# Performance work log

Measured on AMD Instinct MI355X. Metric: run time of the kernel, lower is better.

## Reference

```python
import jax, jax.numpy as jnp
import numpy as np

HID = 2048
HEADS = 16
HD = HID // HEADS  # 128
EPS = 1e-6


def setup_inputs() -> dict:
    key = jax.random.key(0)
    ks = jax.random.split(key, 9)
    s = 1.0 / np.sqrt(HID)
    return {
        "hidden_states": jax.random.normal(ks[0], (4, 4096, HID), jnp.float32),
        "q_w": jax.random.normal(ks[1], (HID, HID), jnp.float32) * s,
        "q_b": jnp.zeros((HID,), jnp.float32),
        "k_w": jax.random.normal(ks[2], (HID, HID), jnp.float32) * s,
        "k_b": jnp.zeros((HID,), jnp.float32),
        "v_w": jax.random.normal(ks[3], (HID, HID), jnp.float32) * s,
        "v_b": jnp.zeros((HID,), jnp.float32),
        "o_w": jax.random.normal(ks[4], (HID, HID), jnp.float32) * s,
        "o_b": jnp.zeros((HID,), jnp.float32),
    }


def _heads(x, b, s):
    # [B,S,HID] -> [B,H,S,Dh]
    return x.reshape(b, s, HEADS, HD).transpose(0, 2, 1, 3)


def reference(hidden_states, q_w, q_b, k_w, k_b, v_w, v_b, o_w, o_b):
    b, s, _ = hidden_states.shape
    # torch Linear: y = x @ W.T + b
    q = _heads(hidden_states @ q_w.T + q_b, b, s)
    k = _heads(hidden_states @ k_w.T + k_b, b, s)
    v = _heads(hidden_states @ v_w.T + v_b, b, s)
    # kernel feature map: elu(x) + 1
    qp = jax.nn.elu(q) + 1.0
    kp = jax.nn.elu(k) + 1.0
    # KV outer-product reduction over sequence: [B,H,Dh,Dh]
    kv = jnp.einsum('bhsd,bhse->bhde', kp, v)
    # normalizer z = q' @ sum_s k'  -> [B,H,S,1]
    z = jnp.einsum('bhsd,bhd->bhs', qp, kp.sum(axis=2))[..., None]
    attn = jnp.einsum('bhsd,bhde->bhse', qp, kv) / (z + EPS)
    out = attn.transpose(0, 2, 1, 3).reshape(b, s, HID)
    return out @ o_w.T + o_b
```

## Files before the change

### kernel.cpp

```cpp
#include <hip/hip_runtime.h>
#include <hip/hip_bf16.h>

#define HIDC 2048
#define NHEADS 16
#define HDIM 128
#define NB 4
#define NS 4096
#define NROWS (NB*NS)
#define QSTR 6144
#define EPSV 1e-6f

typedef __attribute__((ext_vector_type(8))) short s16x8;
typedef __attribute__((ext_vector_type(4))) float f32x4;
typedef __attribute__((ext_vector_type(16))) float f32x16;
typedef __attribute__((ext_vector_type(8))) unsigned short u16x8;

static __device__ __forceinline__ unsigned short f2b(float f) {
  unsigned int u = __float_as_uint(f);
  u += 0x7fffu + ((u >> 16) & 1u);
  return (unsigned short)(u >> 16);
}
static __device__ __forceinline__ float b2f(unsigned short h) {
  return __uint_as_float(((unsigned int)h) << 16);
}

static __device__ __forceinline__ void gload_lds16(const unsigned short* g, unsigned short* l) {
  __builtin_amdgcn_global_load_lds(
      (const __attribute__((address_space(1))) void*)g,
      (__attribute__((address_space(3))) void*)l, 16, 0, 0);
}

__global__ __launch_bounds__(256) void convert_all(
    const float* __restrict__ hs, const float* __restrict__ qw,
    const float* __restrict__ kw, const float* __restrict__ vw,
    const float* __restrict__ ow,
    unsigned short* __restrict__ hsb, unsigned short* __restrict__ qwb,
    unsigned short* __restrict__ kwb, unsigned short* __restrict__ vwb,
    unsigned short* __restrict__ owb)
{
  int bid = blockIdx.x;
  const float* src; unsigned short* dst; size_t base;
  if (bid < 16384) { src = hs; dst = hsb; base = (size_t)bid << 11; }
  else {
    int t = bid - 16384; int wsel = t >> 11; int wb = t & 2047;
    src = wsel == 0 ? qw : wsel == 1 ? kw : wsel == 2 ? vw : ow;
    dst = wsel == 0 ? qwb : wsel == 1 ? kwb : wsel == 2 ? vwb : owb;
    base = (size_t)wb << 11;
  }
  size_t i = base + ((size_t)threadIdx.x << 3);
  float4 a = *(const float4*)(src + i);
  float4 b = *(const float4*)(src + i + 4);
  u16x8 o;
  o[0] = f2b(a.x); o[1] = f2b(a.y); o[2] = f2b(a.z); o[3] = f2b(a.w);
  o[4] = f2b(b.x); o[5] = f2b(b.y); o[6] = f2b(b.z); o[7] = f2b(b.w);
  *(u16x8*)(dst + i) = o;
}

template<int QKV, int OUT_BF16>
__global__ __launch_bounds__(512, 1) void gemm256(
    const unsigned short* __restrict__ A,
    const unsigned short* __restrict__ B0,
    const unsigned short* __restrict__ B1,
    const unsigned short* __restrict__ B2,
    const float* __restrict__ bias0,
    const float* __restrict__ bias1,
    const float* __restrict__ bias2,
    void* __restrict__ Cp,
    int ntile, int astr, int ostr)
{
  __shared__ unsigned short lds[65536];
  const int tid = threadIdx.x;
  const int lane = tid & 63, wid = tid >> 6;
  const int wr = wid >> 2, wc = wid & 3;
  const int l31 = lane & 31, l5 = lane >> 5;

  const int cpx = (int)gridDim.x >> 3;
  const int bidx = (int)blockIdx.x;
  const int wg = (bidx & 7) * cpx + (bidx >> 3);
  const int csz = ntile << 2;
  const int chunk = wg / csz;
  const int tt = wg % csz;
  const int bm = ((chunk << 2) + (tt & 3)) << 8;
  const int bn = (tt >> 2) << 8;

  const unsigned short* Bp = B0;
  const float* bias = bias0;
  bool act = false;
  int bnw = bn;
  if (QKV) {
    int seg = bn >> 11;
    Bp = seg == 0 ? B0 : (seg == 1 ? B1 : B2);
    bias = seg == 0 ? bias0 : (seg == 1 ? bias1 : bias2);
    act = seg < 2;
    bnw = bn & 2047;
  }

  const int r0 = tid >> 2;
  const int s0 = tid & 3;
  const int scol = ((s0 ^ ((r0 >> 3) & 3)) << 3);
  const unsigned short* ApA  = A  + (size_t)(bm  + r0) * astr + scol;
  const unsigned short* ApA2 = ApA + (size_t)128 * astr;
  const unsigned short* BpB  = Bp + (size_t)(bnw + r0) * HIDC + scol;
  const unsigned short* BpB2 = BpB + (size_t)128 * HIDC;

  const int xr = (l31 >> 3) & 3;
  const int sj0 = ((l5 ^ xr) << 3);
  const int sj1 = (((2 + l5) ^ xr) << 3);
  const int abase = ((wr << 7) + l31) * 32;
  const int bbase = 16384 + ((wc << 6) + l31) * 32;

  f32x16 acc[4][2] = {};
  s16x8 a[4][2], b[2][2];

#define LD(off_) (*(const s16x8*)&lds[off_])
#define ST_A(kk_, kt_) { \
    gload_lds16(ApA  + (kt_) + ((kk_) << 5), &lds[wb + ((kk_) << 13) + (tid << 3)]); \
    gload_lds16(ApA2 + (kt_) + ((kk_) << 5), &lds[wb + ((kk_) << 13) + 4096 + (tid << 3)]); }
#define ST_B(kk_, kt_) { \
    gload_lds16(BpB  + (kt_) + ((kk_) << 5), &lds[wb + 16384 + ((kk_) << 13) + (tid << 3)]); \
    gload_lds16(BpB2 + (kt_) + ((kk_) << 5), &lds[wb + 16384 + ((kk_) << 13) + 4096 + (tid << 3)]); }
#define MM8(j_) { \
    acc[0][0] = __builtin_amdgcn_mfma_f32_32x32x16_bf16(a[0][j_], b[0][j_], acc[0][0], 0, 0, 0); \
    acc[0][1] = __builtin_amdgcn_mfma_f32_32x32x16_bf16(a[0][j_], b[1][j_], acc[0][1], 0, 0, 0); \
    acc[1][0] = __builtin_amdgcn_mfma_f32_32x32x16_bf16(a[1][j_], b[0][j_], acc[1][0], 0, 0, 0); \
    acc[1][1] = __builtin_amdgcn_mfma_f32_32x32x16_bf16(a[1][j_], b[1][j_], acc[1][1], 0, 0, 0); \
    acc[2][0] = __builtin_amdgcn_mfma_f32_32x32x16_bf16(a[2][j_], b[0][j_], acc[2][0], 0, 0, 0); \
    acc[2][1] = __builtin_amdgcn_mfma_f32_32x32x16_bf16(a[2][j_], b[1][j_], acc[2][1], 0, 0, 0); \
    acc[3][0] = __builtin_amdgcn_mfma_f32_32x32x16_bf16(a[3][j_], b[0][j_], acc[3][0], 0, 0, 0); \
    acc[3][1] = __builtin_amdgcn_mfma_f32_32x32x16_bf16(a[3][j_], b[1][j_], acc[3][1], 0, 0, 0); }
#define SB   __builtin_amdgcn_sched_barrier(0);
#define BAR  __builtin_amdgcn_s_barrier();
#define PRON __builtin_amdgcn_s_setprio(1);
#define PROFF __builtin_amdgcn_s_setprio(0);

#define PHASE(rb_, kk_, GATE, STG, kts_) { \
    if ((GATE) == 4)      { asm volatile("s_waitcnt vmcnt(4)" ::: "memory"); } \
    else if ((GATE) == 0) { asm volatile("s_waitcnt vmcnt(0)" ::: "memory"); } \
    BAR \
    const int pb = (rb_) + ((kk_) << 13); \
     \
    b[0][0] = LD(pb + bbase + sj0); \
    b[1][0] = LD(pb + bbase + 1024 + sj0); \
    a[0][0] = LD(pb + abase + sj0); \
    a[1][0] = LD(pb + abase + 1024 + sj0); \
    a[2][0] = LD(pb + abase + 2048 + sj0); \
    a[3][0] = LD(pb + abase + 3072 + sj0); \
    if (STG) { ST_A(kk_, kts_); ST_B(kk_, kts_); } \
     \
    b[0][1] = LD(pb + bbase + sj1); \
    b[1][1] = LD(pb + bbase + 1024 + sj1); \
    a[0][1] = LD(pb + abase + sj1); \
    a[1][1] = LD(pb + abase + 1024 + sj1); \
    a[2][1] = LD(pb + abase + 2048 + sj1); \
    a[3][1] = LD(pb + abase + 3072 + sj1); \
    SB PRON MM8(0) MM8(1) PROFF \
  }

  {
    const int wb = 0;
    ST_A(0, 0); ST_B(0, 0);
    ST_A(1, 0); ST_B(1, 0);
  }

  for (int t = 0; t < 31; ++t) {
    const int rb = (t & 1) << 15;
    const int wb = rb ^ 32768;
    const int kts = (t + 1) << 6;
    PHASE(rb, 0, 4, 1, kts)
    PHASE(rb, 1, 4, 1, kts)
  }
  {
    const int rb = (31 & 1) << 15;
    const int wb = 0; (void)wb;
    PHASE(rb, 0, 4, 0, 0)
    PHASE(rb, 1, 0, 0, 0)
  }

#undef PHASE
#undef PROFF
#undef PRON
#undef BAR
#undef SB
#undef MM8
#undef ST_B
#undef ST_A
#undef LD

  #pragma unroll
  for (int mf = 0; mf < 4; ++mf) {
    #pragma unroll
    for (int nf = 0; nf < 2; ++nf) {
      const int colw = (wc << 6) + (nf << 5) + l31;
      const float bv = bias[bnw + colw];
      #pragma unroll
      for (int reg = 0; reg < 16; ++reg) {
        const int row = bm + (wr << 7) + (mf << 5) + (reg & 3) + ((reg >> 2) << 3) + (l5 << 2);
        float v = acc[mf][nf][reg] + bv;
        if (QKV) { if (act) v = (v > 0.f) ? (v + 1.f) : __expf(v); }
        const size_t off = (size_t)row * ostr + bn + colw;
        if (OUT_BF16) ((unsigned short*)Cp)[off] = f2b(v);
        else          ((float*)Cp)[off] = v;
      }
    }
  }
}

__global__ __launch_bounds__(256) void kv_partial(
    const unsigned short* __restrict__ kp, const unsigned short* __restrict__ vv,
    float* __restrict__ kvp, float* __restrict__ ksp)
{
  const int bh = blockIdx.x >> 4;
  const int chunk = blockIdx.x & 15;
  const int b = bh >> 4, h = bh & 15;
  const int tid = threadIdx.x;
  const int td = tid >> 4, te = tid & 15;

  __shared__ float kpl[32][128];
  __shared__ float vl[32][132];

  float acc[8][8] = {};
  float ks[8] = {};

  const size_t rowbase = (size_t)b * NS * QSTR + (size_t)h * HDIM;
  const int s0 = chunk * 256;

  for (int st = 0; st < 256; st += 32) {
    __syncthreads();
    #pragma unroll
    for (int i = 0; i < 2; ++i) {
      int idx = tid + (i << 8);
      int row = idx >> 4, q = idx & 15;
      size_t g = rowbase + (size_t)(s0 + st + row) * QSTR + (q << 3);
      u16x8 k8 = *(const u16x8*)(kp + g);
      u16x8 v8 = *(const u16x8*)(vv + g);
      float tk[8], tv[8];
      #pragma unroll
      for (int j = 0; j < 8; ++j) { tk[j] = b2f(k8[j]); tv[j] = b2f(v8[j]); }
      *(float4*)&kpl[row][(q << 3)]     = make_float4(tk[0], tk[1], tk[2], tk[3]);
      *(float4*)&kpl[row][(q << 3) + 4] = make_float4(tk[4], tk[5], tk[6], tk[7]);
      *(float4*)&vl[row][(q << 3)]      = make_float4(tv[0], tv[1], tv[2], tv[3]);
      *(float4*)&vl[row][(q << 3) + 4]  = make_float4(tv[4], tv[5], tv[6], tv[7]);
    }
    __syncthreads();
    #pragma unroll 4
    for (int s = 0; s < 32; ++s) {
      float kd[8], ve[8];
      *(float4*)&kd[0] = *(const float4*)&kpl[s][td << 3];
      *(float4*)&kd[4] = *(const float4*)&kpl[s][(td << 3) + 4];
      *(float4*)&ve[0] = *(const float4*)&vl[s][te << 3];
      *(float4*)&ve[4] = *(const float4*)&vl[s][(te << 3) + 4];
      if (te == 0) {
        #pragma unroll
        for (int i = 0; i < 8; ++i) ks[i] += kd[i];
      }
      #pragma unroll
      for (int i = 0; i < 8; ++i)
        #pragma unroll
        for (int j = 0; j < 8; ++j)
          acc[i][j] += kd[i] * ve[j];
    }
  }

  float* outp = kvp + ((size_t)(chunk * 64 + bh) << 14);
  #pragma unroll
  for (int j = 0; j < 8; ++j) {
    int e = (te << 3) + j;
    float r0[8];
    #pragma unroll
    for (int i = 0; i < 8; ++i) r0[i] = acc[i][j];
    *(float4*)&outp[(size_t)e * HDIM + (td << 3)]     = *(float4*)&r0[0];
    *(float4*)&outp[(size_t)e * HDIM + (td << 3) + 4] = *(float4*)&r0[4];
  }
  if (te == 0) {
    float* kso = ksp + ((size_t)(chunk * 64 + bh) << 7) + (td << 3);
    #pragma unroll
    for (int i = 0; i < 8; ++i) kso[i] = ks[i];
  }
}

__global__ __launch_bounds__(256) void kv_reduce(
    const float* __restrict__ kvp, float* __restrict__ kvT)
{
  int i = blockIdx.x * 256 + threadIdx.x;
  float s = 0.f;
  #pragma unroll
  for (int c = 0; c < 16; ++c) s += kvp[(size_t)c * (64 * 16384) + i];
  kvT[i] = s;
}

__global__ __launch_bounds__(256) void attn_ker(
    const unsigned short* __restrict__ qp, const float* __restrict__ kvT,
    const float* __restrict__ ksp, unsigned short* __restrict__ attn)
{
  const int bh = blockIdx.x >> 5, stile = blockIdx.x & 31;
  const int b = bh >> 4, h = bh & 15;
  const int tid = threadIdx.x;
  const int lane = tid & 63, w = tid >> 6;
  const int l15 = lane & 15, l4 = lane >> 4;

  __shared__ unsigned short Qs[128][136];
  __shared__ unsigned short Ks[128][136];
  __shared__ float ksl[128];
  __shared__ float zs[128];

  const size_t qbase = ((size_t)b * NS + (size_t)stile * 128) * QSTR + (size_t)h * HDIM;

  #pragma unroll
  for (int i = 0; i < 8; ++i) {
    int idx = tid + (i << 8);
    int row = idx >> 4, q = idx & 15;
    u16x8 v8 = *(const u16x8*)(qp + qbase + (size_t)row * QSTR + (q << 3));
    *(u16x8*)&Qs[row][q << 3] = v8;
  }
  const float* kvb = kvT + ((size_t)bh << 14);
  #pragma unroll
  for (int i = 0; i < 16; ++i) {
    int idx = tid + (i << 8);
    int row = idx >> 5, q = idx & 31;
    float4 v4 = *(const float4*)(kvb + (size_t)row * HDIM + (q << 2));
    ushort4 w4; w4.x = f2b(v4.x); w4.y = f2b(v4.y); w4.z = f2b(v4.z); w4.w = f2b(v4.w);
    *(ushort4*)&Ks[row][q << 2] = w4;
  }
  if (tid < 128) {
    float s = 0.f;
    #pragma unroll
    for (int c = 0; c < 16; ++c) s += ksp[((size_t)(c * 64 + bh) << 7) + tid];
    ksl[tid] = s;
  }
  __syncthreads();
  if (tid < 128) {
    float z = 0.f;
    #pragma unroll
    for (int dq = 0; dq < 16; ++dq) {
      u16x8 qv = *(const u16x8*)&Qs[tid][dq << 3];
      #pragma unroll
      for (int j = 0; j < 8; ++j) z += b2f(qv[j]) * ksl[(dq << 3) + j];
    }
    zs[tid] = 1.f / (z + EPSV);
  }
  __syncthreads();

  f32x4 acc[2][8] = {};
  #pragma unroll
  for (int kk = 0; kk < 4; ++kk) {
    s16x8 a[2], bb[8];
    #pragma unroll
    for (int mf = 0; mf < 2; ++mf)
      a[mf] = *(const s16x8*)&Qs[(w << 5) + (mf << 4) + l15][(kk << 5) + (l4 << 3)];
    #pragma unroll
    for (int nf = 0; nf < 8; ++nf)
      bb[nf] = *(const s16x8*)&Ks[(nf << 4) + l15][(kk << 5) + (l4 << 3)];
    #pragma unroll
    for (int mf = 0; mf < 2; ++mf)
      #pragma unroll
      for (int nf = 0; nf < 8; ++nf)
        acc[mf][nf] = __builtin_amdgcn_mfma_f32_16x16x32_bf16(a[mf], bb[nf], acc[mf][nf], 0, 0, 0);
  }

  #pragma unroll
  for (int mf = 0; mf < 2; ++mf) {
    #pragma unroll
    for (int r = 0; r < 4; ++r) {
      const int rl = (w << 5) + (mf << 4) + (l4 << 2) + r;
      const float zi = zs[rl];
      #pragma unroll
      for (int nf = 0; nf < 8; ++nf) {
        const int e = (nf << 4) + l15;
        attn[qbase + (size_t)rl * QSTR + e] = f2b(acc[mf][nf][r] * zi);
      }
    }
  }
}

extern "C" void kernel_launch(void* const* d_in, const int* in_sizes, int n_in,
                              void* d_out, int out_size, void* d_ws, size_t ws_size,
                              hipStream_t stream) {
  const float* hs = (const float*)d_in[0];
  const float* qw = (const float*)d_in[1];
  const float* qb = (const float*)d_in[2];
  const float* kw = (const float*)d_in[3];
  const float* kb = (const float*)d_in[4];
  const float* vw = (const float*)d_in[5];
  const float* vb = (const float*)d_in[6];
  const float* ow = (const float*)d_in[7];
  const float* ob = (const float*)d_in[8];

  char* w = (char*)d_ws;
  unsigned short* hsb = (unsigned short*)(w);
  unsigned short* qwb = (unsigned short*)(w + 67108864);
  unsigned short* kwb = (unsigned short*)(w + 75497472);
  unsigned short* vwb = (unsigned short*)(w + 83886080);
  unsigned short* owb = (unsigned short*)(w + 92274688);
  unsigned short* qkv = (unsigned short*)(w + 100663296);
  float* kvp = (float*)(w);
  float* ksp = (float*)(w + 67108864);
  float* kvT = (float*)(w + 67108864 + 524288);

  convert_all<<<dim3(24576), dim3(256), 0, stream>>>(hs, qw, kw, vw, ow, hsb, qwb, kwb, vwb, owb);
  gemm256<1, 1><<<dim3(1536), dim3(512), 0, stream>>>(
      hsb, qwb, kwb, vwb, qb, kb, vb, qkv, 24, HIDC, QSTR);
  kv_partial<<<dim3(1024), dim3(256), 0, stream>>>(qkv + 2048, qkv + 4096, kvp, ksp);
  kv_reduce<<<dim3(4096), dim3(256), 0, stream>>>(kvp, kvT);
  attn_ker<<<dim3(2048), dim3(256), 0, stream>>>(qkv, kvT, ksp, qkv + 4096);
  gemm256<0, 0><<<dim3(512), dim3(512), 0, stream>>>(
      qkv + 4096, owb, owb, owb, ob, ob, ob, d_out, 8, QSTR, HIDC);
}
```

Measured before the change: 765.6 us.

## Emit bf16 KV state in reduce and restructure attention kernel with 32x32 MFMA

kv_reduce now writes the summed KV matrix as bf16 and also pre-reduces the per-chunk key sums, so the attention kernel no longer converts fp32 KV or reduces key sums per block. The new attention kernel stages Q into LDS via direct global-to-LDS loads with an XOR swizzle. It reads KV fragments straight from global memory and uses 32x32x16 MFMA tiles on a 2x2 wave grid. The normalizer is computed by two threads per row reading Q from global. This cuts redundant per-block conversion and reduction work and LDS traffic, at the cost of uncoalesced global B-fragment loads and an extra read of Q for z.

```diff
diff --git a/kernel.cpp b/kernel.cpp
--- a/kernel.cpp
+++ b/kernel.cpp
@@ -138,7 +138,6 @@
     else if ((GATE) == 0) { asm volatile("s_waitcnt vmcnt(0)" ::: "memory"); } \
     BAR \
     const int pb = (rb_) + ((kk_) << 13); \
-     \
     b[0][0] = LD(pb + bbase + sj0); \
     b[1][0] = LD(pb + bbase + 1024 + sj0); \
     a[0][0] = LD(pb + abase + sj0); \
@@ -146,7 +145,6 @@
     a[2][0] = LD(pb + abase + 2048 + sj0); \
     a[3][0] = LD(pb + abase + 3072 + sj0); \
     if (STG) { ST_A(kk_, kts_); ST_B(kk_, kts_); } \
-     \
     b[0][1] = LD(pb + bbase + sj1); \
     b[1][1] = LD(pb + bbase + 1024 + sj1); \
     a[0][1] = LD(pb + abase + sj1); \
@@ -279,28 +277,37 @@
 }
 
 __global__ __launch_bounds__(256) void kv_reduce(
-    const float* __restrict__ kvp, float* __restrict__ kvT)
+    const float* __restrict__ kvp, unsigned short* __restrict__ kvTb,
+    const float* __restrict__ ksp, float* __restrict__ ksumf)
 {
   int i = blockIdx.x * 256 + threadIdx.x;
   float s = 0.f;
   #pragma unroll
   for (int c = 0; c < 16; ++c) s += kvp[(size_t)c * (64 * 16384) + i];
-  kvT[i] = s;
-}
-
-__global__ __launch_bounds__(256) void attn_ker(
-    const unsigned short* __restrict__ qp, const float* __restrict__ kvT,
-    const float* __restrict__ ksp, unsigned short* __restrict__ attn)
+  kvTb[i] = f2b(s);
+  if (blockIdx.x < 32) {
+    int j = blockIdx.x * 256 + threadIdx.x;
+    float t = 0.f;
+    #pragma unroll
+    for (int c = 0; c < 16; ++c) t += ksp[c * 8192 + j];
+    ksumf[j] = t;
+  }
+}
+
+__global__ __launch_bounds__(256) void attn2(
+    const unsigned short* __restrict__ qp, const unsigned short* __restrict__ kvTb,
+    const float* __restrict__ ksumf, unsigned short* __restrict__ attn)
 {
   const int bh = blockIdx.x >> 5, stile = blockIdx.x & 31;
   const int b = bh >> 4, h = bh & 15;
   const int tid = threadIdx.x;
-  const int lane = tid & 63, w = tid >> 6;
-  const int l15 = lane & 15, l4 = lane >> 4;
-
-  __shared__ unsigned short Qs[128][136];
-  __shared__ unsigned short Ks[128][136];
+  const int lane = tid & 63, wid = tid >> 6;
+  const int wr = wid >> 1, wc = wid & 1;
+  const int l31 = lane & 31, l5 = lane >> 5;
+
+  __shared__ unsigned short qs[16384];
   __shared__ float ksl[128];
+  __shared__ float zsh[256];
   __shared__ float zs[128];
 
   const size_t qbase = ((size_t)b * NS + (size_t)stile * 128) * QSTR + (size_t)h * HDIM;
@@ -308,65 +315,60 @@
   #pragma unroll
   for (int i = 0; i < 8; ++i) {
     int idx = tid + (i << 8);
-    int row = idx >> 4, q = idx & 15;
-    u16x8 v8 = *(const u16x8*)(qp + qbase + (size_t)row * QSTR + (q << 3));
-    *(u16x8*)&Qs[row][q << 3] = v8;
-  }
-  const float* kvb = kvT + ((size_t)bh << 14);
-  #pragma unroll
-  for (int i = 0; i < 16; ++i) {
-    int idx = tid + (i << 8);
-    int row = idx >> 5, q = idx & 31;
-    float4 v4 = *(const float4*)(kvb + (size_t)row * HDIM + (q << 2));
-    ushort4 w4; w4.x = f2b(v4.x); w4.y = f2b(v4.y); w4.z = f2b(v4.z); w4.w = f2b(v4.w);
-    *(ushort4*)&Ks[row][q << 2] = w4;
-  }
-  if (tid < 128) {
-    float s = 0.f;
-    #pragma unroll
-    for (int c = 0; c < 16; ++c) s += ksp[((size_t)(c * 64 + bh) << 7) + tid];
-    ksl[tid] = s;
+    int r = idx >> 4, s = idx & 15;
+    gload_lds16(qp + qbase + (size_t)r * QSTR + ((s ^ (r & 15)) << 3), &qs[idx << 3]);
+  }
+  if (tid < 32) {
+    *(float4*)&ksl[tid << 2] = *(const float4*)(ksumf + (bh << 7) + (tid << 2));
   }
   __syncthreads();
-  if (tid < 128) {
-    float z = 0.f;
-    #pragma unroll
-    for (int dq = 0; dq < 16; ++dq) {
-      u16x8 qv = *(const u16x8*)&Qs[tid][dq << 3];
+
+  {
+    const int row = tid >> 1, half = tid & 1;
+    const unsigned short* qr = qp + qbase + (size_t)row * QSTR + (half << 6);
+    float zp = 0.f;
+    #pragma unroll
+    for (int q8 = 0; q8 < 8; ++q8) {
+      u16x8 v8 = *(const u16x8*)(qr + (q8 << 3));
       #pragma unroll
-      for (int j = 0; j < 8; ++j) z += b2f(qv[j]) * ksl[(dq << 3) + j];
+      for (int j = 0; j < 8; ++j) zp += b2f(v8[j]) * ksl[(half << 6) + (q8 << 3) + j];
     }
-    zs[tid] = 1.f / (z + EPSV);
+    zsh[tid] = zp;
   }
   __syncthreads();
-
-  f32x4 acc[2][8] = {};
-  #pragma unroll
-  for (int kk = 0; kk < 4; ++kk) {
-    s16x8 a[2], bb[8];
-    #pragma unroll
-    for (int mf = 0; mf < 2; ++mf)
-      a[mf] = *(const s16x8*)&Qs[(w << 5) + (mf << 4) + l15][(kk << 5) + (l4 << 3)];
-    #pragma unroll
-    for (int nf = 0; nf < 8; ++nf)
-      bb[nf] = *(const s16x8*)&Ks[(nf << 4) + l15][(kk << 5) + (l4 << 3)];
-    #pragma unroll
-    for (int mf = 0; mf < 2; ++mf)
+  if ((tid & 1) == 0) {
+    const int row = tid >> 1;
+    zs[row] = 1.f / (zsh[tid] + zsh[tid + 1] + EPSV);
+  }
+  __syncthreads();
+
+  f32x16 acc[2][2] = {};
+  const unsigned short* kvb = kvTb + ((size_t)bh << 14);
+  const unsigned short* bp0 = kvb + (((wc << 6) + l31) << 7) + (l5 << 3);
+  const int ar0 = (wr << 6) + l31;
+  const int ar1 = ar0 + 32;
+  #pragma unroll
+  for (int kk = 0; kk < 8; ++kk) {
+    const int sN = (kk << 1) + l5;
+    s16x8 a0 = *(const s16x8*)&qs[(ar0 << 7) + ((sN ^ (ar0 & 15)) << 3)];
+    s16x8 a1 = *(const s16x8*)&qs[(ar1 << 7) + ((sN ^ (ar1 & 15)) << 3)];
+    s16x8 b0 = *(const s16x8*)(bp0 + (kk << 4));
+    s16x8 b1 = *(const s16x8*)(bp0 + 4096 + (kk << 4));
+    acc[0][0] = __builtin_amdgcn_mfma_f32_32x32x16_bf16(a0, b0, acc[0][0], 0, 0, 0);
+    acc[0][1] = __builtin_amdgcn_mfma_f32_32x32x16_bf16(a0, b1, acc[0][1], 0, 0, 0);
+    acc[1][0] = __builtin_amdgcn_mfma_f32_32x32x16_bf16(a1, b0, acc[1][0], 0, 0, 0);
+    acc[1][1] = __builtin_amdgcn_mfma_f32_32x32x16_bf16(a1, b1, acc[1][1], 0, 0, 0);
+  }
+
+  #pragma unroll
+  for (int mf = 0; mf < 2; ++mf) {
+    #pragma unroll
+    for (int nf = 0; nf < 2; ++nf) {
+      const int e = (wc << 6) + (nf << 5) + l31;
       #pragma unroll
-      for (int nf = 0; nf < 8; ++nf)
-        acc[mf][nf] = __builtin_amdgcn_mfma_f32_16x16x32_bf16(a[mf], bb[nf], acc[mf][nf], 0, 0, 0);
-  }
-
-  #pragma unroll
-  for (int mf = 0; mf < 2; ++mf) {
-    #pragma unroll
-    for (int r = 0; r < 4; ++r) {
-      const int rl = (w << 5) + (mf << 4) + (l4 << 2) + r;
-      const float zi = zs[rl];
-      #pragma unroll
-      for (int nf = 0; nf < 8; ++nf) {
-        const int e = (nf << 4) + l15;
-        attn[qbase + (size_t)rl * QSTR + e] = f2b(acc[mf][nf][r] * zi);
+      for (int reg = 0; reg < 16; ++reg) {
+        const int row = (wr << 6) + (mf << 5) + (reg & 3) + ((reg >> 2) << 3) + (l5 << 2);
+        attn[qbase + (size_t)row * QSTR + e] = f2b(acc[mf][nf][reg] * zs[row]);
       }
     }
   }
@@ -394,14 +396,15 @@
   unsigned short* qkv = (unsigned short*)(w + 100663296);
   float* kvp = (float*)(w);
   float* ksp = (float*)(w + 67108864);
-  float* kvT = (float*)(w + 67108864 + 524288);
+  unsigned short* kvTb = (unsigned short*)(w + 67108864 + 524288);
+  float* ksumf = (float*)(w + 67108864 + 524288 + 2097152);
 
   convert_all<<<dim3(24576), dim3(256), 0, stream>>>(hs, qw, kw, vw, ow, hsb, qwb, kwb, vwb, owb);
   gemm256<1, 1><<<dim3(1536), dim3(512), 0, stream>>>(
       hsb, qwb, kwb, vwb, qb, kb, vb, qkv, 24, HIDC, QSTR);
   kv_partial<<<dim3(1024), dim3(256), 0, stream>>>(qkv + 2048, qkv + 4096, kvp, ksp);
-  kv_reduce<<<dim3(4096), dim3(256), 0, stream>>>(kvp, kvT);
-  attn_ker<<<dim3(2048), dim3(256), 0, stream>>>(qkv, kvT, ksp, qkv + 4096);
+  kv_reduce<<<dim3(4096), dim3(256), 0, stream>>>(kvp, kvTb, ksp, ksumf);
+  attn2<<<dim3(2048), dim3(256), 0, stream>>>(qkv, kvTb, ksumf, qkv + 4096);
   gemm256<0, 0><<<dim3(512), dim3(512), 0, stream>>>(
       qkv + 4096, owb, owb, owb, ob, ob, ob, d_out, 8, QSTR, HIDC);
 }
```

After: 771.9 us. About the same (+0.8%).
